# Performance work log

Hardware: AMD Instinct MI355X
Metric: run time of the kernel (lower is better)

## Reference

```python
import jax, jax.numpy as jnp
import numpy as np

N, E, MUL, ATTR, NBASIS = 30000, 480000, 32, 8, 8
AVG_NEIGH = 16.0
INV_SQRT3 = 1.0 / np.sqrt(3.0).astype(np.float32)  # wigner 3j (1,1,0)
LOG2 = float(np.log(2.0))


def ssp(x):
    # shifted softplus: softplus(x) - log(2)
    return jax.nn.softplus(x) - LOG2


def setup_inputs() -> dict:
    key = jax.random.key(0)
    ks = jax.random.split(key, 15)
    return {
        "node_s": jax.random.normal(ks[0], (N, MUL), jnp.float32),
        "node_v": jax.random.normal(ks[1], (N, MUL, 3), jnp.float32),
        "node_attr": jax.random.uniform(ks[2], (N, ATTR), jnp.float32),
        "edge_attr": jax.random.normal(ks[3], (E, 4), jnp.float32),       # [sh0 | sh1(3)]
        "edge_scalars": jax.random.uniform(ks[4], (E, NBASIS), jnp.float32),
        "W1_0": jax.random.normal(ks[5], (MUL, MUL), jnp.float32),
        "W1_1": jax.random.normal(ks[6], (MUL, MUL), jnp.float32),
        "Wfc1": jax.random.normal(ks[7], (NBASIS, NBASIS), jnp.float32),
        "Wfc2": jax.random.normal(ks[8], (NBASIS, 4 * MUL), jnp.float32),
        "W2_0": jax.random.normal(ks[9], (2 * MUL, MUL), jnp.float32),
        "W2_1": jax.random.normal(ks[10], (2 * MUL, MUL), jnp.float32),
        "Wsc0": jax.random.normal(ks[11], (MUL, ATTR, MUL), jnp.float32),
        "Wsc1": jax.random.normal(ks[12], (MUL, ATTR, MUL), jnp.float32),
        "edge_src": jax.random.randint(ks[13], (E,), 0, N, jnp.int32),
        "edge_dst": jax.random.randint(ks[14], (E,), 0, N, jnp.int32),
    }


def reference(node_s, node_v, node_attr, edge_attr, edge_scalars,
              W1_0, W1_1, Wfc1, Wfc2, W2_0, W2_1, Wsc0, Wsc1,
              edge_src, edge_dst):
    n_nodes, mul = node_s.shape
    # --- fc: radial MLP -> per-edge TP weights (shared_weights=False) ---
    h = ssp(edge_scalars @ Wfc1 * (1.0 / np.sqrt(Wfc1.shape[0])))
    w = h @ Wfc2 * (1.0 / np.sqrt(Wfc2.shape[0]))                 # [E, 4*MUL]
    w00, w01, w10, w11 = jnp.split(w, 4, axis=1)                  # instruction order
    # --- lin1: per-irrep linear (fan-in normalized) ---
    inv_m = 1.0 / np.sqrt(mul)
    x0 = node_s @ W1_0 * inv_m                                    # [N, MUL]
    x1 = jnp.einsum('nud,uw->nwd', node_v, W1_1) * inv_m          # [N, MUL, 3]
    # --- gather destination-node features per edge ---
    x0d, x1d = x0[edge_dst], x1[edge_dst]
    sh0, sh1 = edge_attr[:, :1], edge_attr[:, 1:4]
    # --- uvu tensor product with per-edge weights ---
    s_a = w00 * x0d * sh0                                         # 0e x 0e -> 0e
    s_b = w11 * jnp.einsum('eud,ed->eu', x1d, sh1) * INV_SQRT3    # 1o x 1o -> 0e
    v_a = (w01 * x0d)[:, :, None] * sh1[:, None, :]               # 0e x 1o -> 1o
    v_b = w10[:, :, None] * x1d * sh0[:, :, None]                 # 1o x 0e -> 1o
    mid_s = jnp.concatenate([s_a, s_b], axis=1)                   # [E, 64]  (64x0e)
    mid_v = jnp.concatenate([v_a, v_b], axis=1)                   # [E, 64, 3] (64x1o)
    # --- scatter-sum over edge_src, normalized by sqrt(avg_num_neighbors) ---
    inv_nb = 1.0 / np.sqrt(AVG_NEIGH)
    agg_s = jax.ops.segment_sum(mid_s, edge_src, num_segments=n_nodes) * inv_nb
    agg_v = jax.ops.segment_sum(mid_v, edge_src, num_segments=n_nodes) * inv_nb
    # --- lin2 ---
    inv_2m = 1.0 / np.sqrt(2.0 * mul)
    out0 = agg_s @ W2_0 * inv_2m                                  # [N, MUL]
    out1 = jnp.einsum('nud,uw->nwd', agg_v, W2_1) * inv_2m        # [N, MUL, 3]
    # --- self-connection: fully-connected TP (attr is scalar 8x0e) ---
    sc_norm = 1.0 / np.sqrt(mul * node_attr.shape[1])
    sc0 = jnp.einsum('nu,nv,uvw->nw', node_s, node_attr, Wsc0) * sc_norm
    sc1 = jnp.einsum('nud,nv,uvw->nwd', node_v, node_attr, Wsc1) * sc_norm
    o0 = out0 + sc0
    o1 = out1 + sc1
    return jnp.concatenate([o0, o1.reshape(n_nodes, mul * 3)], axis=1)  # [N, 128]
```

## Files before the change

### kernel.cpp

```cpp
#include <hip/hip_runtime.h>
#include <math.h>

#define N_NODES 30000
#define N_EDGES 480000

typedef __attribute__((ext_vector_type(8))) short short8;
typedef __attribute__((ext_vector_type(4))) float f32x4;
typedef __attribute__((ext_vector_type(2))) float f32x2;

__device__ __forceinline__ unsigned short f2bf(float f) {
    unsigned u = __float_as_uint(f);
    u += 0x7fff + ((u >> 16) & 1);
    return (unsigned short)(u >> 16);
}
__device__ __forceinline__ float bfLO(unsigned v) { return __uint_as_float(v << 16); }
__device__ __forceinline__ float bfHI(unsigned v) { return __uint_as_float(v & 0xffff0000u); }
__device__ __forceinline__ unsigned packbf(float a, float b) {
    return (unsigned)f2bf(a) | ((unsigned)f2bf(b) << 16);
}
__device__ __forceinline__ unsigned ptk(float a, float b) {
    return (__float_as_uint(a) >> 16) | (__float_as_uint(b) & 0xffff0000u);
}

union U8 { short8 v; unsigned u[4]; };
union C4 { f32x4 v; float f[4]; };

__global__ __launch_bounds__(256) void k_pre(
    const float* __restrict__ node_s,
    const float* __restrict__ node_v,
    const float* __restrict__ W1_0,
    const float* __restrict__ W1_1,
    const float* __restrict__ Wsc0,
    const float* __restrict__ Wsc1,
    const float* __restrict__ W2_0,
    const float* __restrict__ W2_1,
    const int* __restrict__ edge_src,
    int* __restrict__ deg,
    unsigned short* __restrict__ xnode,
    unsigned* __restrict__ bsc0,
    unsigned* __restrict__ bsc1,
    unsigned* __restrict__ b20,
    unsigned* __restrict__ b21)
{
    __shared__ float sVT[16 * 100];
    __shared__ float sXo[16 * 140];
    int tid = threadIdx.x;

    if (blockIdx.x >= 1875) {
        int b = blockIdx.x - 1875;
        const float* Wm = (b == 0) ? Wsc0 : (b == 1) ? Wsc1 : (b == 2) ? W2_0 : W2_1;
        unsigned* dst = (b == 0) ? bsc0 : (b == 1) ? bsc1 : (b == 2) ? b20 : b21;
        float scale = (b < 2) ? 0.0625f : 0.03125f;
        int nu = (b < 2) ? 4096 : 1024;
        for (int idx = tid; idx < nu; idx += 256) {
            int jp = idx & 3;
            int lane = (idx >> 2) & 63;
            int ft = (idx >> 8) & 1;
            int kc = idx >> 9;
            int quad = lane >> 4, col = lane & 15;
            int k = kc * 32 + quad * 8 + jp * 2;
            int c = ft * 16 + col;
            dst[idx] = packbf(Wm[k * 32 + c] * scale, Wm[(k + 1) * 32 + c] * scale);
        }
        return;
    }

    atomicAdd(&deg[edge_src[blockIdx.x * 256 + tid]], 1);

    int nbase = blockIdx.x * 16;
    for (int i = tid; i < 1536; i += 256) {
        int nl = i / 96, r = i - nl * 96;
        int u = r / 3, d = r - u * 3;
        sVT[nl * 100 + d * 32 + u] = node_v[(size_t)nbase * 96 + i];
    }
    __syncthreads();

    int lane = tid & 63;
    int wv = tid >> 6;
    int col = lane & 15, quad = lane >> 4, m = lane & 15;

    const float* W1 = (wv == 0) ? W1_0 : W1_1;
    U8 bf0, bf1;
#pragma unroll
    for (int p = 0; p < 4; ++p) {
        int k = quad * 8 + 2 * p;
        bf0.u[p] = packbf(W1[k * 32 + col],      W1[(k + 1) * 32 + col]);
        bf1.u[p] = packbf(W1[k * 32 + col + 16], W1[(k + 1) * 32 + col + 16]);
    }

    U8 af;
    if (wv == 0) {
        const float* sp = node_s + (size_t)(nbase + m) * 32 + quad * 8;
        float4 a0 = *(const float4*)(sp);
        float4 a1 = *(const float4*)(sp + 4);
        af.u[0] = packbf(a0.x, a0.y); af.u[1] = packbf(a0.z, a0.w);
        af.u[2] = packbf(a1.x, a1.y); af.u[3] = packbf(a1.z, a1.w);
    } else {
        int R = 16 * (wv - 1) + m;
        int nl = R / 3, d = R - nl * 3;
        const float* vp = sVT + nl * 100 + d * 32 + quad * 8;
        af.u[0] = packbf(vp[0], vp[1]); af.u[1] = packbf(vp[2], vp[3]);
        af.u[2] = packbf(vp[4], vp[5]); af.u[3] = packbf(vp[6], vp[7]);
    }

    f32x4 acc0 = {0.f, 0.f, 0.f, 0.f};
    f32x4 acc1 = {0.f, 0.f, 0.f, 0.f};
    acc0 = __builtin_amdgcn_mfma_f32_16x16x32_bf16(af.v, bf0.v, acc0, 0, 0, 0);
    acc1 = __builtin_amdgcn_mfma_f32_16x16x32_bf16(af.v, bf1.v, acc1, 0, 0, 0);

    C4 c0, c1;
    c0.v = acc0; c1.v = acc1;
    if (wv == 0) {
#pragma unroll
        for (int r = 0; r < 4; ++r) {
            int nl = (quad << 2) + r;
            sXo[nl * 140 + col]      = c0.f[r];
            sXo[nl * 140 + col + 16] = c1.f[r];
        }
    } else {
#pragma unroll
        for (int r = 0; r < 4; ++r) {
            int R = 16 * (wv - 1) + (quad << 2) + r;
            int nl = R / 3, d = R - nl * 3;
            sXo[nl * 140 + (1 + d) * 34 + col]      = c0.f[r];
            sXo[nl * 140 + (1 + d) * 34 + col + 16] = c1.f[r];
        }
    }
    __syncthreads();

    const float inv_m = 0.1767766953f;
    for (int i = tid; i < 512; i += 256) {
        int nl = i >> 5, u = i & 31;
        const float* xp = sXo + nl * 140;
        uint2 pk;
        pk.x = packbf(xp[u] * inv_m,       xp[34 + u] * inv_m);
        pk.y = packbf(xp[68 + u] * inv_m,  xp[102 + u] * inv_m);
        *(uint2*)(xnode + (size_t)(nbase + nl) * 128 + u * 4) = pk;
    }
}

__global__ __launch_bounds__(1024) void scan_kernel(const int* __restrict__ deg,
                                                    int* __restrict__ offs,
                                                    int* __restrict__ cursor) {
    __shared__ int sdeg[N_NODES];
    __shared__ int wsum[16];
    int tid = threadIdx.x;
#pragma unroll
    for (int k = 0; k < 30; ++k) {
        int idx = k * 1024 + tid;
        if (idx < N_NODES) sdeg[idx] = deg[idx];
    }
    __syncthreads();
    int base = tid * 30;
    int s = 0;
    if (base < N_NODES) {
#pragma unroll
        for (int k = 0; k < 30; ++k) s += sdeg[base + k];
    }
    int lane = tid & 63, wid = tid >> 6;
    int inc = s;
#pragma unroll
    for (int d = 1; d < 64; d <<= 1) {
        int o = __shfl_up(inc, d, 64);
        if (lane >= d) inc += o;
    }
    if (lane == 63) wsum[wid] = inc;
    __syncthreads();
    if (tid < 16) {
        int v = wsum[tid];
        int t = v;
#pragma unroll
        for (int d = 1; d < 16; d <<= 1) {
            int o = __shfl_up(t, d, 64);
            if (tid >= d) t += o;
        }
        wsum[tid] = t - v;
    }
    __syncthreads();
    int run = inc - s + wsum[wid];
    if (base < N_NODES) {
#pragma unroll
        for (int k = 0; k < 30; ++k) {
            int n = base + k;
            int d = sdeg[n];
            sdeg[n] = run;
            run += d;
        }
    }
    __syncthreads();
#pragma unroll
    for (int k = 0; k < 30; ++k) {
        int idx = k * 1024 + tid;
        if (idx < N_NODES) {
            int v = sdeg[idx];
            offs[idx] = v;
            cursor[idx] = v;
        }
    }
    if (tid == 0) offs[N_NODES] = N_EDGES;
}

__global__ __launch_bounds__(256) void fill_kernel(
    const float* __restrict__ edge_attr,
    const float* __restrict__ edge_scalars,
    const float* __restrict__ Wfc1,
    const int* __restrict__ edge_src,
    const int* __restrict__ edge_dst,
    int* __restrict__ cursor,
    uint4* __restrict__ rec)
{
    __shared__ float sW[64];
    int tid = threadIdx.x;
    if (tid < 64) sW[tid] = Wfc1[tid];
    __syncthreads();

    int e = blockIdx.x * 256 + tid;
    float4 es0 = *(const float4*)(edge_scalars + (size_t)e * 8);
    float4 es1 = *(const float4*)(edge_scalars + (size_t)e * 8 + 4);
    float4 ea  = *(const float4*)(edge_attr + (size_t)e * 4);
    int src = edge_src[e];
    int dst = edge_dst[e];
    int pos = atomicAdd(&cursor[src], 1);

    const float inv8 = 0.3535533906f;
    float h[8];
#pragma unroll
    for (int i = 0; i < 8; ++i) {
        float acc = es0.x * sW[0 * 8 + i];
        acc = fmaf(es0.y, sW[1 * 8 + i], acc);
        acc = fmaf(es0.z, sW[2 * 8 + i], acc);
        acc = fmaf(es0.w, sW[3 * 8 + i], acc);
        acc = fmaf(es1.x, sW[4 * 8 + i], acc);
        acc = fmaf(es1.y, sW[5 * 8 + i], acc);
        acc = fmaf(es1.z, sW[6 * 8 + i], acc);
        acc = fmaf(es1.w, sW[7 * 8 + i], acc);
        acc *= inv8;
        float ax = fabsf(acc);
        float tt = __expf(-ax);
        h[i] = fmaxf(acc, 0.f) + __logf(1.f + tt) - 0.6931471806f;
    }
    uint4 r0, r1;
    r0.x = packbf(h[0], h[1]); r0.y = packbf(h[2], h[3]);
    r0.z = packbf(h[4], h[5]); r0.w = packbf(h[6], h[7]);
    r1.x = packbf(ea.x, ea.y); r1.y = packbf(ea.z, ea.w);
    r1.z = ((unsigned)dst) << 8;
    r1.w = 0;
    rec[2 * pos]     = r0;
    rec[2 * pos + 1] = r1;
}

struct GAcc {
    float sa, sb, va2, vb2;
    f32x2 va01, vb01;
};

__device__ __forceinline__ void gstep(
    uint4& RS0, uint4& RS1, uint2& XS, const uint4& RN1, uint2& XN,
    int& t, int cntH, int& pf, int L,
    const char* recc, const char* xbc,
    const f32x2* wfA, const f32x2* wfB, GAcc& g)
{
    float hv[8];
    hv[0] = bfLO(RS0.x); hv[1] = bfHI(RS0.x);
    hv[2] = bfLO(RS0.y); hv[3] = bfHI(RS0.y);
    hv[4] = bfLO(RS0.z); hv[5] = bfHI(RS0.z);
    hv[6] = bfLO(RS0.w); hv[7] = bfHI(RS0.w);
    float sh0  = bfLO(RS1.x), s1xe = bfHI(RS1.x);
    float s1ye = bfLO(RS1.y), s1ze = bfHI(RS1.y);
    float xv0 = bfLO(XS.x), xd0 = bfHI(XS.x);
    float xd1 = bfLO(XS.y), xd2 = bfHI(XS.y);
    bool ok = (t < cntH);

    RS0 = *(const uint4*)(recc + pf);
    RS1 = *(const uint4*)(recc + pf + 16);
    pf = min(pf + 64, L);
    XN = *(const uint2*)(xbc + RN1.z);

    f32x2 aA = {0.f, 0.f}, aB = {0.f, 0.f};
#pragma unroll
    for (int q = 0; q < 8; ++q) {
        f32x2 hh = {hv[q], hv[q]};
        aA = __builtin_elementwise_fma(hh, wfA[q], aA);
        aB = __builtin_elementwise_fma(hh, wfB[q], aB);
    }
    float a00 = ok ? aA.x : 0.f;
    float a01 = ok ? aA.y : 0.f;
    float a10 = ok ? aB.x : 0.f;
    float a11 = ok ? aB.y : 0.f;

    float dot = xd0 * s1xe + xd1 * s1ye + xd2 * s1ze;
    g.sa = fmaf(a00 * sh0, xv0, g.sa);
    g.sb = fmaf(a11, dot, g.sb);
    float w01x0 = a01 * xv0;
    float t10 = a10 * sh0;
    f32x2 wb = {w01x0, w01x0};
    f32x2 tb = {t10, t10};
    f32x2 s01 = {s1xe, s1ye};
    f32x2 xd01 = {xd0, xd1};
    g.va01 = __builtin_elementwise_fma(wb, s01, g.va01);
    g.vb01 = __builtin_elementwise_fma(tb, xd01, g.vb01);
    g.va2 = fmaf(w01x0, s1ze, g.va2);
    g.vb2 = fmaf(t10, xd2, g.vb2);
    ++t;
}

__global__ __launch_bounds__(256, 5) void k_gather(
    const int* __restrict__ offs,
    const uint4* __restrict__ rec,
    const float* __restrict__ Wfc2,
    const unsigned short* __restrict__ xnode,
    unsigned short* __restrict__ agg)
{
    __shared__ float sWf[1024];
    int tid = threadIdx.x;
    const float inv8 = 0.3535533906f;
    const float inv_s3 = 0.5773502692f;
    for (int i = tid; i < 1024; i += 256) {
        float sc = ((i & 127) >= 96) ? inv8 * inv_s3 : inv8;
        sWf[i] = Wfc2[i] * sc;
    }
    __syncthreads();

    int lane = tid & 63;
    int u = lane & 31;
    int half = lane >> 5;
    int wv = tid >> 6;
    int node = blockIdx.x * 4 + wv;

    f32x2 wfA[8], wfB[8];
#pragma unroll
    for (int q = 0; q < 8; ++q) {
        const float* wp = sWf + q * 128 + u;
        wfA[q].x = wp[0];  wfA[q].y = wp[32];
        wfB[q].x = wp[64]; wfB[q].y = wp[96];
    }

    int beg = offs[node], end = offs[node + 1];
    int cnt = end - beg;

    GAcc g;
    g.sa = 0.f; g.sb = 0.f; g.va2 = 0.f; g.vb2 = 0.f;
    g.va01 = (f32x2){0.f, 0.f};
    g.vb01 = (f32x2){0.f, 0.f};

    if (cnt > 0) {
        const char* recc = (const char*)rec;
        const char* xbc  = (const char*)xnode + u * 8;
        int T = (cnt + 1) >> 1;
        int cntH = (cnt + 1 - half) >> 1;
        int L = (end - 1) * 32;
        int b0 = (beg + half) * 32;

        uint4 r00, r01, r10, r11, r20, r21;
        uint2 x0, x1, x2;
        x2.x = 0u; x2.y = 0u;
        int p;
        p = min(b0, L);        r00 = *(const uint4*)(recc + p); r01 = *(const uint4*)(recc + p + 16);
        p = min(b0 + 64, L);   r10 = *(const uint4*)(recc + p); r11 = *(const uint4*)(recc + p + 16);
        p = min(b0 + 128, L);  r20 = *(const uint4*)(recc + p); r21 = *(const uint4*)(recc + p + 16);
        int pf = min(b0 + 192, L);
        x0 = *(const uint2*)(xbc + r01.z);
        x1 = *(const uint2*)(xbc + r11.z);

        int t = 0;
        int Tm = T - 2;
        while (t < Tm) {
            gstep(r00, r01, x0, r21, x2, t, cntH, pf, L, recc, xbc, wfA, wfB, g);
            gstep(r10, r11, x1, r01, x0, t, cntH, pf, L, recc, xbc, wfA, wfB, g);
            gstep(r20, r21, x2, r11, x1, t, cntH, pf, L, recc, xbc, wfA, wfB, g);
        }
        if (t < T) gstep(r00, r01, x0, r21, x2, t, cntH, pf, L, recc, xbc, wfA, wfB, g);
        if (t < T) gstep(r10, r11, x1, r01, x0, t, cntH, pf, L, recc, xbc, wfA, wfB, g);
    }

    g.sa      += __shfl_xor(g.sa, 32, 64);
    g.sb      += __shfl_xor(g.sb, 32, 64);
    g.va01.x  += __shfl_xor(g.va01.x, 32, 64);
    g.va01.y  += __shfl_xor(g.va01.y, 32, 64);
    g.vb01.x  += __shfl_xor(g.vb01.x, 32, 64);
    g.vb01.y  += __shfl_xor(g.vb01.y, 32, 64);
    g.va2     += __shfl_xor(g.va2, 32, 64);
    g.vb2     += __shfl_xor(g.vb2, 32, 64);

    unsigned short* ap = agg + (size_t)node * 256;
    if (half == 0) {
        ap[u]       = f2bf(g.sa);
        ap[32 + u]  = f2bf(g.sb);
        ap[64 + u]  = f2bf(g.va01.x);
        ap[96 + u]  = f2bf(g.vb01.x);
    } else {
        ap[128 + u] = f2bf(g.va01.y);
        ap[160 + u] = f2bf(g.vb01.y);
        ap[192 + u] = f2bf(g.va2);
        ap[224 + u] = f2bf(g.vb2);
    }
}

__global__ __launch_bounds__(256) void k_gemm(
    const unsigned short* agg,
    const float* __restrict__ node_s,
    const float* __restrict__ node_v,
    const float* __restrict__ node_attr,
    const unsigned* __restrict__ bsc0,
    const unsigned* __restrict__ bsc1,
    const unsigned* __restrict__ b20,
    const unsigned* __restrict__ b21,
    float* out)
{
    __shared__ float sS[16 * 33];
    __shared__ float sV[16 * 100];
    int tid = threadIdx.x;
    int lane = tid & 63;
    int wv = tid >> 6;
    int nbase = blockIdx.x * 16;

    for (int i = tid; i < 512; i += 256)
        sS[(i >> 5) * 33 + (i & 31)] = node_s[(size_t)nbase * 32 + i];
    for (int i = tid; i < 1536; i += 256)
        sV[(i / 96) * 100 + (i % 96)] = node_v[(size_t)nbase * 96 + i];

    int col = lane & 15;
    int quad = lane >> 4;
    int m = col;
    bool is_s = (wv == 0);
    int sub = wv - 1;

    const short* Bs = (const short*)(is_s ? bsc0 : bsc1);
    const short* B2 = (const short*)(is_s ? b20 : b21);

    int aBase, fbase, fstep, n_a;
    if (is_s) {
        aBase = m * 256;
        fbase = m * 33;
        fstep = 1;
        n_a = nbase + m;
    } else {
        int r16 = 16 * sub + m;
        int nl = r16 / 3;
        int dd = r16 - nl * 3;
        aBase = nl * 256 + 64 + 64 * dd;
        fbase = nl * 100 + dd;
        fstep = 3;
        n_a = nbase + nl;
    }

    const short* aggp = (const short*)agg + (size_t)nbase * 256 + aBase + quad * 8;
    short8 afW0 = *(const short8*)(aggp);
    short8 afW1 = *(const short8*)(aggp + 32);

    float4 A0 = *(const float4*)(node_attr + (size_t)n_a * 8);
    float4 A1 = *(const float4*)(node_attr + (size_t)n_a * 8 + 4);
    float aa0 = A0.x, aa1 = A0.y, aa2 = A0.z, aa3 = A0.w;
    float aa4 = A1.x, aa5 = A1.y, aa6 = A1.z, aa7 = A1.w;

    __syncthreads();

    f32x4 acc0 = {0.f, 0.f, 0.f, 0.f};
    f32x4 acc1 = {0.f, 0.f, 0.f, 0.f};

    {
        short8 bf0 = *(const short8*)(B2 + (0 * 64 + lane) * 8);
        short8 bf1 = *(const short8*)(B2 + (1 * 64 + lane) * 8);
        acc0 = __builtin_amdgcn_mfma_f32_16x16x32_bf16(afW0, bf0, acc0, 0, 0, 0);
        acc1 = __builtin_amdgcn_mfma_f32_16x16x32_bf16(afW0, bf1, acc1, 0, 0, 0);
        bf0 = *(const short8*)(B2 + (2 * 64 + lane) * 8);
        bf1 = *(const short8*)(B2 + (3 * 64 + lane) * 8);
        acc0 = __builtin_amdgcn_mfma_f32_16x16x32_bf16(afW1, bf0, acc0, 0, 0, 0);
        acc1 = __builtin_amdgcn_mfma_f32_16x16x32_bf16(afW1, bf1, acc1, 0, 0, 0);
    }

    const float* Sf = is_s ? sS : sV;
#pragma unroll
    for (int kc = 0; kc < 8; ++kc) {
        int uu = kc * 4 + quad;
        float f = Sf[fbase + uu * fstep];
        U8 af;
        af.u[0] = ptk(f * aa0, f * aa1);
        af.u[1] = ptk(f * aa2, f * aa3);
        af.u[2] = ptk(f * aa4, f * aa5);
        af.u[3] = ptk(f * aa6, f * aa7);
        short8 bf0 = *(const short8*)(Bs + ((kc * 2 + 0) * 64 + lane) * 8);
        short8 bf1 = *(const short8*)(Bs + ((kc * 2 + 1) * 64 + lane) * 8);
        acc0 = __builtin_amdgcn_mfma_f32_16x16x32_bf16(af.v, bf0, acc0, 0, 0, 0);
        acc1 = __builtin_amdgcn_mfma_f32_16x16x32_bf16(af.v, bf1, acc1, 0, 0, 0);
    }

    C4 c0, c1;
    c0.v = acc0; c1.v = acc1;
    if (is_s) {
#pragma unroll
        for (int r = 0; r < 4; ++r) {
            int n = nbase + (quad << 2) + r;
            out[(size_t)n * 128 + col]      = c0.f[r];
            out[(size_t)n * 128 + col + 16] = c1.f[r];
        }
    } else {
#pragma unroll
        for (int r = 0; r < 4; ++r) {
            int rl = 16 * sub + (quad << 2) + r;
            int nn = rl / 3;
            int dd = rl - nn * 3;
            int n = nbase + nn;
            out[(size_t)n * 128 + 32 + 3 * col + dd]        = c0.f[r];
            out[(size_t)n * 128 + 32 + 3 * (col + 16) + dd] = c1.f[r];
        }
    }
}

extern "C" void kernel_launch(void* const* d_in, const int* in_sizes, int n_in,
                              void* d_out, int out_size, void* d_ws, size_t ws_size,
                              hipStream_t stream) {
    const float* node_s       = (const float*)d_in[0];
    const float* node_v       = (const float*)d_in[1];
    const float* node_attr    = (const float*)d_in[2];
    const float* edge_attr    = (const float*)d_in[3];
    const float* edge_scalars = (const float*)d_in[4];
    const float* W1_0 = (const float*)d_in[5];
    const float* W1_1 = (const float*)d_in[6];
    const float* Wfc1 = (const float*)d_in[7];
    const float* Wfc2 = (const float*)d_in[8];
    const float* W2_0 = (const float*)d_in[9];
    const float* W2_1 = (const float*)d_in[10];
    const float* Wsc0 = (const float*)d_in[11];
    const float* Wsc1 = (const float*)d_in[12];
    const int* edge_src = (const int*)d_in[13];
    const int* edge_dst = (const int*)d_in[14];

    char* ws = (char*)d_ws;
    unsigned short* xnode = (unsigned short*)(ws);
    uint4* rec            = (uint4*)(ws + 7680000);
    int* deg    = (int*)(ws + 23040000);
    int* offs   = (int*)(ws + 23160000);
    int* cursor = (int*)(ws + 23280016);
    unsigned* bsc0 = (unsigned*)(ws + 23400064);
    unsigned* bsc1 = (unsigned*)(ws + 23416448);
    unsigned* b20  = (unsigned*)(ws + 23432832);
    unsigned* b21  = (unsigned*)(ws + 23436928);

    hipMemsetAsync(deg, 0, (size_t)N_NODES * sizeof(int), stream);
    k_pre<<<1879, 256, 0, stream>>>(node_s, node_v, W1_0, W1_1, Wsc0, Wsc1,
                                    W2_0, W2_1, edge_src, deg, xnode,
                                    bsc0, bsc1, b20, b21);
    scan_kernel<<<1, 1024, 0, stream>>>(deg, offs, cursor);
    fill_kernel<<<1875, 256, 0, stream>>>(edge_attr, edge_scalars, Wfc1,
                                          edge_src, edge_dst, cursor, rec);
    k_gather<<<7500, 256, 0, stream>>>(offs, rec, Wfc2, xnode,
                                       (unsigned short*)d_out);
    k_gemm<<<1875, 256, 0, stream>>>((const unsigned short*)d_out,
                                     node_s, node_v, node_attr,
                                     bsc0, bsc1, b20, b21, (float*)d_out);
}
```

Before: 238.3 us.

## Deepen gather prefetch pipeline to six stages and drop shared-memory Wfc2 staging

The edge gather loop now keeps six edge records in flight with node-feature loads issued four steps ahead, up from three and two. The goal is to hide more global memory latency per wave. Wfc2 weights now load directly from global memory into registers, which removes the shared-memory staging and the block barrier. The occupancy hint in launch_bounds is also dropped. The extra registers may lower occupancy, and the tail handling must still cover every edge.

```diff
diff --git a/kernel.cpp b/kernel.cpp
--- a/kernel.cpp
+++ b/kernel.cpp
@@ -304,35 +304,30 @@
     ++t;
 }
 
-__global__ __launch_bounds__(256, 5) void k_gather(
+__global__ __launch_bounds__(256) void k_gather(
     const int* __restrict__ offs,
     const uint4* __restrict__ rec,
     const float* __restrict__ Wfc2,
     const unsigned short* __restrict__ xnode,
     unsigned short* __restrict__ agg)
 {
-    __shared__ float sWf[1024];
     int tid = threadIdx.x;
-    const float inv8 = 0.3535533906f;
-    const float inv_s3 = 0.5773502692f;
-    for (int i = tid; i < 1024; i += 256) {
-        float sc = ((i & 127) >= 96) ? inv8 * inv_s3 : inv8;
-        sWf[i] = Wfc2[i] * sc;
-    }
-    __syncthreads();
-
     int lane = tid & 63;
     int u = lane & 31;
     int half = lane >> 5;
     int wv = tid >> 6;
     int node = blockIdx.x * 4 + wv;
 
+    const float inv8 = 0.3535533906f;
+    const float i8s3 = 0.3535533906f * 0.5773502692f;
     f32x2 wfA[8], wfB[8];
 #pragma unroll
     for (int q = 0; q < 8; ++q) {
-        const float* wp = sWf + q * 128 + u;
-        wfA[q].x = wp[0];  wfA[q].y = wp[32];
-        wfB[q].x = wp[64]; wfB[q].y = wp[96];
+        const float* wp = Wfc2 + q * 128 + u;
+        wfA[q].x = wp[0]  * inv8;
+        wfA[q].y = wp[32] * inv8;
+        wfB[q].x = wp[64] * inv8;
+        wfB[q].y = wp[96] * i8s3;
     }
 
     int beg = offs[node], end = offs[node + 1];
@@ -351,26 +346,37 @@
         int L = (end - 1) * 32;
         int b0 = (beg + half) * 32;
 
-        uint4 r00, r01, r10, r11, r20, r21;
-        uint2 x0, x1, x2;
-        x2.x = 0u; x2.y = 0u;
+        uint4 r00, r01, r10, r11, r20, r21, r30, r31, r40, r41, r50, r51;
+        uint2 x0, x1, x2, x3, x4, x5;
+        x4.x = 0u; x4.y = 0u; x5.x = 0u; x5.y = 0u;
         int p;
-        p = min(b0, L);        r00 = *(const uint4*)(recc + p); r01 = *(const uint4*)(recc + p + 16);
-        p = min(b0 + 64, L);   r10 = *(const uint4*)(recc + p); r11 = *(const uint4*)(recc + p + 16);
-        p = min(b0 + 128, L);  r20 = *(const uint4*)(recc + p); r21 = *(const uint4*)(recc + p + 16);
-        int pf = min(b0 + 192, L);
+        p = min(b0,       L); r00 = *(const uint4*)(recc + p); r01 = *(const uint4*)(recc + p + 16);
+        p = min(b0 + 64,  L); r10 = *(const uint4*)(recc + p); r11 = *(const uint4*)(recc + p + 16);
+        p = min(b0 + 128, L); r20 = *(const uint4*)(recc + p); r21 = *(const uint4*)(recc + p + 16);
+        p = min(b0 + 192, L); r30 = *(const uint4*)(recc + p); r31 = *(const uint4*)(recc + p + 16);
+        p = min(b0 + 256, L); r40 = *(const uint4*)(recc + p); r41 = *(const uint4*)(recc + p + 16);
+        p = min(b0 + 320, L); r50 = *(const uint4*)(recc + p); r51 = *(const uint4*)(recc + p + 16);
+        int pf = min(b0 + 384, L);
         x0 = *(const uint2*)(xbc + r01.z);
         x1 = *(const uint2*)(xbc + r11.z);
+        x2 = *(const uint2*)(xbc + r21.z);
+        x3 = *(const uint2*)(xbc + r31.z);
 
         int t = 0;
-        int Tm = T - 2;
+        int Tm = T - 5;
         while (t < Tm) {
-            gstep(r00, r01, x0, r21, x2, t, cntH, pf, L, recc, xbc, wfA, wfB, g);
-            gstep(r10, r11, x1, r01, x0, t, cntH, pf, L, recc, xbc, wfA, wfB, g);
-            gstep(r20, r21, x2, r11, x1, t, cntH, pf, L, recc, xbc, wfA, wfB, g);
-        }
-        if (t < T) gstep(r00, r01, x0, r21, x2, t, cntH, pf, L, recc, xbc, wfA, wfB, g);
-        if (t < T) gstep(r10, r11, x1, r01, x0, t, cntH, pf, L, recc, xbc, wfA, wfB, g);
+            gstep(r00, r01, x0, r41, x4, t, cntH, pf, L, recc, xbc, wfA, wfB, g);
+            gstep(r10, r11, x1, r51, x5, t, cntH, pf, L, recc, xbc, wfA, wfB, g);
+            gstep(r20, r21, x2, r01, x0, t, cntH, pf, L, recc, xbc, wfA, wfB, g);
+            gstep(r30, r31, x3, r11, x1, t, cntH, pf, L, recc, xbc, wfA, wfB, g);
+            gstep(r40, r41, x4, r21, x2, t, cntH, pf, L, recc, xbc, wfA, wfB, g);
+            gstep(r50, r51, x5, r31, x3, t, cntH, pf, L, recc, xbc, wfA, wfB, g);
+        }
+        if (t < T) gstep(r00, r01, x0, r41, x4, t, cntH, pf, L, recc, xbc, wfA, wfB, g);
+        if (t < T) gstep(r10, r11, x1, r51, x5, t, cntH, pf, L, recc, xbc, wfA, wfB, g);
+        if (t < T) gstep(r20, r21, x2, r01, x0, t, cntH, pf, L, recc, xbc, wfA, wfB, g);
+        if (t < T) gstep(r30, r31, x3, r11, x1, t, cntH, pf, L, recc, xbc, wfA, wfB, g);
+        if (t < T) gstep(r40, r41, x4, r21, x2, t, cntH, pf, L, recc, xbc, wfA, wfB, g);
     }
 
     g.sa      += __shfl_xor(g.sa, 32, 64);
```

New measurement: 236.2 us. About the same (-0.9%).
